# Optimization experiments

Hardware: AMD Instinct MI355X
Metric: run time of the kernel (lower is better)

Reference implementation:

```python
import jax, jax.numpy as jnp
import numpy as np

NUM_GROUPS = 32
EPS = 1e-6


def group_norm(x, gamma, beta):
    # x: [B, C, H, W]; GroupNorm over (channels-in-group, H, W)
    B, C, H, W = x.shape
    xg = x.reshape(B, NUM_GROUPS, C // NUM_GROUPS, H, W)
    mean = xg.mean(axis=(2, 3, 4), keepdims=True)
    var = xg.var(axis=(2, 3, 4), keepdims=True)
    xn = ((xg - mean) * jax.lax.rsqrt(var + EPS)).reshape(B, C, H, W)
    return xn * gamma[None, :, None, None] + beta[None, :, None, None]


def conv1x1(x, w, b):
    # 1x1 conv == channel-mixing matmul. w: [C_out, C_in]
    return jnp.einsum('bchw,oc->bohw', x, w) + b[None, :, None, None]


def setup_inputs() -> dict:
    key = jax.random.key(0)
    ks = jax.random.split(key, 6)
    B, C, H, W = 8, 256, 64, 64
    s = 1.0 / np.sqrt(C)  # fan-in scaled weights (like Conv2d default)
    inp = {
        'x': jax.random.normal(ks[0], (B, C, H, W), jnp.float32),
        'gamma': jnp.ones((C,), jnp.float32),
        'beta': jnp.zeros((C,), jnp.float32),
        'wq': jax.random.normal(ks[1], (C, C), jnp.float32) * s,
        'bq': jnp.zeros((C,), jnp.float32),
        'wk': jax.random.normal(ks[2], (C, C), jnp.float32) * s,
        'bk': jnp.zeros((C,), jnp.float32),
        'wv': jax.random.normal(ks[3], (C, C), jnp.float32) * s,
        'bv': jnp.zeros((C,), jnp.float32),
        'wo': jax.random.normal(ks[4], (C, C), jnp.float32) * s,
        'bo': jnp.zeros((C,), jnp.float32),
    }
    return inp


def reference(x, gamma, beta, wq, bq, wk, bk, wv, bv, wo, bo):
    B, C, H, W = x.shape
    h = group_norm(x, gamma, beta)
    q = conv1x1(h, wq, bq)
    k = conv1x1(h, wk, bk)
    v = conv1x1(h, wv, bv)
    # elu + 1 feature map (nonnegative kernel features)
    q = jax.nn.elu(q) + 1.0
    k = jax.nn.elu(k) + 1.0
    N = H * W
    kf = k.reshape(B, C, N)            # [B, C, N]
    vf = v.reshape(B, C, N)            # [B, C, N]
    qf = q.reshape(B, C, N)            # [B, C, N]
    # kv = k @ v^T : [B, C, C]
    kv = jnp.einsum('bcn,bdn->bcd', kf, vf)
    # h_out[b, n, d] = sum_c q[b, c, n] * kv[b, c, d]; stored channel-first
    h_out = jnp.einsum('bcn,bcd->bdn', qf, kv).reshape(B, C, H, W)
    return x + conv1x1(h_out, wo, bo)
```

## Files before the change

### kernel.cpp

```cpp
#include <hip/hip_runtime.h>
#include <math.h>

#define C_DIM 256
#define N_DIM 4096
#define B_DIM 8

typedef __attribute__((ext_vector_type(8))) short bf16x8;
typedef __attribute__((ext_vector_type(4))) float f32x4;
typedef __attribute__((ext_vector_type(8))) unsigned short us8;
typedef __attribute__((ext_vector_type(4))) unsigned short us4;

__device__ inline unsigned short f2bf(float f) {
    unsigned int u = __float_as_uint(f);
    u += 0x7fffu + ((u >> 16) & 1u);
    return (unsigned short)(u >> 16);
}

__device__ inline void gload_lds16(const void* g, void* l) {
    __builtin_amdgcn_global_load_lds(
        (const __attribute__((address_space(1))) unsigned int*)g,
        (__attribute__((address_space(3))) unsigned int*)l, 16, 0, 0);
}

__global__ __launch_bounds__(256) void prep_kernel(
    const float* __restrict__ wq, const float* __restrict__ wk,
    const float* __restrict__ wv, const float* __restrict__ wo,
    const float* __restrict__ bk, const float* __restrict__ bv,
    const float* __restrict__ x,
    unsigned short* __restrict__ wqb, unsigned short* __restrict__ wkvb,
    unsigned short* __restrict__ wob, float* __restrict__ bkv,
    float2* __restrict__ sums)
{
    int z = blockIdx.x;
    int t = threadIdx.x;
    if (z < 256) {
        const float* s; unsigned short* d;
        int which = z >> 6;
        if (which == 0)      { s = wq; d = wqb; }
        else if (which == 1) { s = wk; d = wkvb; }
        else if (which == 2) { s = wv; d = wkvb + 65536; }
        else                 { s = wo; d = wob; }
        int idx = (z & 63) * 1024 + t * 4;
        float4 v = *(const float4*)(s + idx);
        us4 r; r[0] = f2bf(v.x); r[1] = f2bf(v.y); r[2] = f2bf(v.z); r[3] = f2bf(v.w);
        *(us4*)(d + idx) = r;
    } else if (z == 256) {
        bkv[t]       = bk[t];
        bkv[t + 256] = bv[t];
    } else {
        int bc = z - 257;
        const float* xc = x + (size_t)bc * N_DIM;
        float s = 0.f, q = 0.f;
        for (int i = t; i < 1024; i += 256) {
            float4 v = ((const float4*)xc)[i];
            s += v.x + v.y + v.z + v.w;
            q += v.x*v.x + v.y*v.y + v.z*v.z + v.w*v.w;
        }
        #pragma unroll
        for (int off = 32; off > 0; off >>= 1) {
            s += __shfl_down(s, off);
            q += __shfl_down(q, off);
        }
        __shared__ float red[8];
        int w = t >> 6;
        if ((t & 63) == 0) { red[w*2] = s; red[w*2+1] = q; }
        __syncthreads();
        if (t == 0) {
            sums[bc] = make_float2(red[0]+red[2]+red[4]+red[6],
                                   red[1]+red[3]+red[5]+red[7]);
        }
    }
}

__global__ __launch_bounds__(256) void kvred(const float* __restrict__ src, unsigned short* __restrict__ dst) {
    int gi = (blockIdx.x * 256 + threadIdx.x) * 4;
    int b = gi >> 16, idx = gi & 65535;
    float4 a = make_float4(0.f,0.f,0.f,0.f);
    #pragma unroll
    for (int sp = 0; sp < 8; sp++) {
        float4 v = *(const float4*)(src + (((size_t)b*8 + sp) << 16) + idx);
        a.x += v.x; a.y += v.y; a.z += v.z; a.w += v.w;
    }
    us4 r; r[0] = f2bf(a.x); r[1] = f2bf(a.y); r[2] = f2bf(a.z); r[3] = f2bf(a.w);
    *(us4*)(dst + ((size_t)b << 16) + idx) = r;
}


__device__ __forceinline__ void stage_w(const unsigned short* __restrict__ W,
                                        unsigned short* __restrict__ dst, int kt, int t) {
    #pragma unroll
    for (int s = 0; s < 4; s++) {
        int c = t + s*256;
        int row = c >> 2, slot = c & 3;
        int cs = slot ^ ((row >> 1) & 3);
        gload_lds16(W + (size_t)row*256 + kt + cs*8, dst + c*8);
    }
}

__device__ __forceinline__ void phase_kv(
    const unsigned short* __restrict__ W, const unsigned short* __restrict__ hs,
    unsigned short* __restrict__ wst, unsigned short* __restrict__ kvdst,
    const float* __restrict__ biasr, int ccb, int n0, bool elu, int t)
{
    int w = t >> 6, l = t & 63;
    int wm = w >> 1, wn = w & 1;
    int l15 = l & 15, quad = l >> 4;
    int acol = (quad ^ ((l15 >> 1) & 3)) * 8;
    int rsw  = (l15 >> 1) & 3;

    f32x4 acc[8][2];
    #pragma unroll
    for (int i = 0; i < 8; i++)
        #pragma unroll
        for (int j = 0; j < 2; j++)
            #pragma unroll
            for (int r = 0; r < 4; r++) acc[i][j][r] = 0.f;

    stage_w(W, wst, 0, t);
    asm volatile("s_waitcnt vmcnt(0)" ::: "memory");
    __syncthreads();

    int buf = 0;
    for (int kt = 0; kt < 8; ++kt) {
        if (kt + 1 < 8) stage_w(W, wst + (buf^1)*8192, (kt+1)*32, t);
        __builtin_amdgcn_sched_barrier(0);
        bf16x8 af[8], bfr[2];
        #pragma unroll
        for (int i = 0; i < 8; i++)
            af[i] = *(const bf16x8*)(wst + buf*8192 + (wm*128 + i*16 + l15)*32 + acol);
        #pragma unroll
        for (int j = 0; j < 2; j++) {
            int n = wn*32 + j*16 + l15;
            bfr[j] = *(const bf16x8*)(hs + n*256 + (kt*4 + (quad ^ rsw))*8);
        }
        __builtin_amdgcn_s_setprio(1);
        #pragma unroll
        for (int i = 0; i < 8; i++)
            #pragma unroll
            for (int j = 0; j < 2; j++)
                acc[i][j] = __builtin_amdgcn_mfma_f32_16x16x32_bf16(af[i], bfr[j], acc[i][j], 0, 0, 0);
        __builtin_amdgcn_s_setprio(0);
        __builtin_amdgcn_sched_barrier(0);
        asm volatile("s_waitcnt vmcnt(0)" ::: "memory");
        __syncthreads();
        buf ^= 1;
    }

    unsigned short* ep = wst;
    #pragma unroll
    for (int h = 0; h < 2; h++) {
        if (wm == h) {
            #pragma unroll
            for (int i = 0; i < 8; i++) {
                #pragma unroll
                for (int j = 0; j < 2; j++) {
                    int cl = wn*32 + j*16 + l15;
                    #pragma unroll
                    for (int r = 0; r < 4; r++) {
                        int rloc = i*16 + quad*4 + r;
                        float val = acc[i][j][r] + biasr[h*128 + rloc];
                        if (elu) val = val > 0.f ? val + 1.f : __expf(val);
                        ep[rloc*72 + cl] = f2bf(val);
                    }
                }
            }
        }
        __syncthreads();
        #pragma unroll
        for (int it = 0; it < 4; it++) {
            int idx = t + it*256;
            int row = idx >> 3;
            int colc = (idx & 7) * 8;
            us8 vv = *(us8*)(ep + row*72 + colc);
            *(us8*)(kvdst + (size_t)(ccb + h*128 + row)*4096 + n0 + colc) = vv;
        }
        __syncthreads();
    }
}

__device__ __forceinline__ void phase_q(
    const unsigned short* __restrict__ W, const unsigned short* __restrict__ hs,
    unsigned short* __restrict__ wst, unsigned short* __restrict__ qdst,
    const float* __restrict__ bq, int n0, int t)
{
    int w = t >> 6, l = t & 63;
    int wm = w >> 1, wn = w & 1;
    int l15 = l & 15, quad = l >> 4;
    int acol = (quad ^ ((l15 >> 1) & 3)) * 8;
    int rsw  = (l15 >> 1) & 3;

    f32x4 acc[2][8];
    #pragma unroll
    for (int i = 0; i < 2; i++)
        #pragma unroll
        for (int j = 0; j < 8; j++)
            #pragma unroll
            for (int r = 0; r < 4; r++) acc[i][j][r] = 0.f;

    stage_w(W, wst, 0, t);
    asm volatile("s_waitcnt vmcnt(0)" ::: "memory");
    __syncthreads();

    int buf = 0;
    for (int kt = 0; kt < 8; ++kt) {
        if (kt + 1 < 8) stage_w(W, wst + (buf^1)*8192, (kt+1)*32, t);
        __builtin_amdgcn_sched_barrier(0);
        bf16x8 af[2], bfr[8];
        #pragma unroll
        for (int i = 0; i < 2; i++) {
            int n = wm*32 + i*16 + l15;
            af[i] = *(const bf16x8*)(hs + n*256 + (kt*4 + (quad ^ rsw))*8);
        }
        #pragma unroll
        for (int j = 0; j < 8; j++)
            bfr[j] = *(const bf16x8*)(wst + buf*8192 + (wn*128 + j*16 + l15)*32 + acol);
        __builtin_amdgcn_s_setprio(1);
        #pragma unroll
        for (int i = 0; i < 2; i++)
            #pragma unroll
            for (int j = 0; j < 8; j++)
                acc[i][j] = __builtin_amdgcn_mfma_f32_16x16x32_bf16(af[i], bfr[j], acc[i][j], 0, 0, 0);
        __builtin_amdgcn_s_setprio(0);
        __builtin_amdgcn_sched_barrier(0);
        asm volatile("s_waitcnt vmcnt(0)" ::: "memory");
        __syncthreads();
        buf ^= 1;
    }

    unsigned short* ep = wst;
    #pragma unroll
    for (int h = 0; h < 2; h++) {
        if (wm == h) {
            #pragma unroll
            for (int i = 0; i < 2; i++) {
                #pragma unroll
                for (int j = 0; j < 8; j++) {
                    int cl = wn*128 + j*16 + l15;
                    float bi = bq[cl];
                    #pragma unroll
                    for (int r = 0; r < 4; r++) {
                        int rloc = i*16 + quad*4 + r;
                        float val = acc[i][j][r] + bi;
                        val = val > 0.f ? val + 1.f : __expf(val);
                        ep[rloc*264 + cl] = f2bf(val);
                    }
                }
            }
        }
        __syncthreads();
        #pragma unroll
        for (int it = 0; it < 4; it++) {
            int idx = t + it*256;
            int row = idx >> 5;
            int colc = (idx & 31) * 8;
            us8 vv = *(us8*)(ep + row*264 + colc);
            *(us8*)(qdst + (size_t)(n0 + h*32 + row)*256 + colc) = vv;
        }
        __syncthreads();
    }
}

__global__ __launch_bounds__(256, 2) void fused_qkv(
    const float* __restrict__ x, const float2* __restrict__ sums,
    const float* __restrict__ gamma, const float* __restrict__ beta,
    const unsigned short* __restrict__ wqb, const unsigned short* __restrict__ wkvb,
    const float* __restrict__ bq, const float* __restrict__ bkv,
    unsigned short* __restrict__ qT, unsigned short* __restrict__ kvbuf)
{
    __shared__ __align__(16) unsigned short hs[16384];
    __shared__ __align__(16) unsigned short wst[16384];
    __shared__ float scale[256], shift[256];

    int b  = blockIdx.y;
    int n0 = blockIdx.x * 64;
    int t  = threadIdx.x;

    {
        int c = t, gbase = c & ~7;
        float s = 0.f, q = 0.f;
        #pragma unroll
        for (int j = 0; j < 8; j++) { float2 u = sums[b*256 + gbase + j]; s += u.x; q += u.y; }
        float mean = s * (1.f/32768.f);
        float var  = q * (1.f/32768.f) - mean*mean;
        float inv  = rsqrtf(var + 1e-6f);
        float gm = gamma[c] * inv;
        scale[c] = gm; shift[c] = beta[c] - mean*gm;
    }
    __syncthreads();

    #pragma unroll
    for (int it = 0; it < 8; ++it) {
        int c  = it*32 + (t >> 3);
        int nl = (t & 7) * 8;
        const float* xp = x + ((size_t)(b*256 + c))*4096 + n0 + nl;
        float4 v0 = *(const float4*)xp;
        float4 v1 = *(const float4*)(xp + 4);
        float sc = scale[c], sh = shift[c];
        int chunk = c >> 3, pos = c & 7;
        float vv[8] = {v0.x, v0.y, v0.z, v0.w, v1.x, v1.y, v1.z, v1.w};
        #pragma unroll
        for (int r = 0; r < 8; ++r) {
            int n = nl + r;
            int cs = (chunk & ~3) | ((chunk & 3) ^ ((n >> 1) & 3));
            hs[n*256 + cs*8 + pos] = f2bf(vv[r] * sc + sh);
        }
    }
    __syncthreads();

    unsigned short* kvdst = kvbuf + (size_t)b * 2097152;
    phase_kv(wkvb,         hs, wst, kvdst, bkv,       0,   n0, true,  t);
    phase_kv(wkvb + 65536, hs, wst, kvdst, bkv + 256, 256, n0, false, t);
    phase_q (wqb,          hs, wst, qT + (size_t)b*1048576, bq, n0, t);
}

template<int MODE>
__device__ __forceinline__ void gemm_body(
    const unsigned short* __restrict__ Ab, const unsigned short* __restrict__ Bb,
    const float* __restrict__ bias, const float* __restrict__ residb,
    void* __restrict__ Cb,
    int N, int K, int k0, int Ks, int m_blk, int n_blk, char* smem)
{
    unsigned short* lds = (unsigned short*)smem;

    int t = threadIdx.x;
    int w = t >> 6, l = t & 63;
    int wm = w >> 1, wn = w & 1;
    int l15 = l & 15, quad = l >> 4;

    int srow = w * 16 + (l >> 2);
    int skc  = (((l & 3) ^ ((l >> 3) & 3)) * 8);

    f32x4 acc[4][4];
    #pragma unroll
    for (int i = 0; i < 4; i++)
        #pragma unroll
        for (int j = 0; j < 4; j++)
            #pragma unroll
            for (int r = 0; r < 4; r++) acc[i][j][r] = 0.f;

    auto stage = [&](int buf, int kt) {
        unsigned short* Asl = lds + buf*8192 + t*8;
        unsigned short* Bsl = Asl + 4096;
        #pragma unroll
        for (int rep = 0; rep < 2; rep++) {
            gload_lds16(Ab + (size_t)(m_blk + rep*64 + srow) * K + kt + skc, Asl + rep*2048);
            gload_lds16(Bb + (size_t)(n_blk + rep*64 + srow) * K + kt + skc, Bsl + rep*2048);
        }
    };

    const int nt = Ks >> 5;

    stage(0, k0);
    if (nt > 1) stage(1, k0 + 32);

    int acol = (quad ^ ((l15 >> 1) & 3)) * 8;

    int bufc = 0;
    for (int kt = 0; kt < nt; ++kt) {
        if (kt + 1 < nt) asm volatile("s_waitcnt vmcnt(4)" ::: "memory");
        else             asm volatile("s_waitcnt vmcnt(0)" ::: "memory");
        __builtin_amdgcn_s_barrier();
        __builtin_amdgcn_sched_barrier(0);
        if (kt + 2 < nt) {
            int bufn = bufc + 2; if (bufn >= 3) bufn -= 3;
            stage(bufn, k0 + (kt + 2) * 32);
        }
        __builtin_amdgcn_sched_barrier(0);

        const unsigned short* Aw = lds + bufc*8192 + (wm*64 + l15)*32 + acol;
        const unsigned short* Bw = lds + bufc*8192 + 4096 + (wn*64 + l15)*32 + acol;
        bf16x8 af[4], bfr[4];
        #pragma unroll
        for (int i = 0; i < 4; i++) af[i]  = *(const bf16x8*)(Aw + i*512);
        #pragma unroll
        for (int j = 0; j < 4; j++) bfr[j] = *(const bf16x8*)(Bw + j*512);
        __builtin_amdgcn_s_setprio(1);
        #pragma unroll
        for (int i = 0; i < 4; i++)
            #pragma unroll
            for (int j = 0; j < 4; j++)
                acc[i][j] = __builtin_amdgcn_mfma_f32_16x16x32_bf16(af[i], bfr[j], acc[i][j], 0, 0, 0);
        __builtin_amdgcn_s_setprio(0);
        bufc = (bufc == 2) ? 0 : bufc + 1;
    }
    __syncthreads();

    if (MODE == 4) {
        unsigned short* ep = (unsigned short*)smem;
        unsigned short* Cp = (unsigned short*)Cb;
        #pragma unroll
        for (int h = 0; h < 2; h++) {
            if (wm == h) {
                int row0 = quad*4;
                int col0 = wn*64 + l15;
                #pragma unroll
                for (int i = 0; i < 4; i++)
                    #pragma unroll
                    for (int j = 0; j < 4; j++)
                        #pragma unroll
                        for (int r = 0; r < 4; r++)
                            ep[(row0 + i*16 + r)*136 + col0 + j*16] = f2bf(acc[i][j][r]);
            }
            __syncthreads();
            #pragma unroll
            for (int it = 0; it < 4; it++) {
                int row = it*16 + (t >> 4);
                int col = (t & 15) * 8;
                us8 vv = *(us8*)(ep + row*136 + col);
                *(us8*)(Cp + (size_t)(m_blk + h*64 + row) * N + n_blk + col) = vv;
            }
            __syncthreads();
        }
    } else {
        float* ep32 = (float*)smem;
        float* Cp = (float*)Cb;
        #pragma unroll
        for (int h = 0; h < 2; h++) {
            if (wm == h) {
                int row0 = quad*4;
                int col0 = wn*64 + l15;
                #pragma unroll
                for (int i = 0; i < 4; i++)
                    #pragma unroll
                    for (int j = 0; j < 4; j++)
                        #pragma unroll
                        for (int r = 0; r < 4; r++)
                            ep32[(row0 + i*16 + r)*140 + col0 + j*16] = acc[i][j][r];
            }
            __syncthreads();
            #pragma unroll
            for (int it = 0; it < 8; it++) {
                int rl  = it*8 + (t >> 5);
                int row = m_blk + h*64 + rl;
                int col = (t & 31) * 4;
                f32x4 vv = *(f32x4*)(ep32 + rl*140 + col);
                if (MODE == 5) {
                    float bi = bias[row];
                    float4 rv = *(const float4*)(residb + (size_t)row * N + n_blk + col);
                    vv[0] += bi + rv.x; vv[1] += bi + rv.y;
                    vv[2] += bi + rv.z; vv[3] += bi + rv.w;
                }
                *(f32x4*)(Cp + (size_t)row * N + n_blk + col) = vv;
            }
            __syncthreads();
        }
    }
}

template<int MODE>
__global__ __launch_bounds__(256) void gemm_nt(
    const unsigned short* __restrict__ A, const unsigned short* __restrict__ B,
    const float* __restrict__ bias, const float* __restrict__ resid,
    void* __restrict__ Cout,
    int N, int K, int splits,
    size_t sA, size_t sB, size_t sC, size_t sR, int elem4)
{
    __shared__ __align__(16) char smem[49152];
    int b  = blockIdx.z / splits;
    int sp = blockIdx.z % splits;
    int Ks = K / splits;
    size_t cbase = (MODE == 3) ? ((size_t)(b*splits + sp)) * sC : (size_t)b * sC;
    void* Cb = elem4 ? (void*)((float*)Cout + cbase) : (void*)((unsigned short*)Cout + cbase);
    gemm_body<MODE>(A + b*sA, B + b*sB, bias,
                    resid ? resid + b*sR : nullptr, Cb,
                    N, K, sp*Ks, Ks, blockIdx.y*128, blockIdx.x*128, smem);
}

extern "C" void kernel_launch(void* const* d_in, const int* in_sizes, int n_in,
                              void* d_out, int out_size, void* d_ws, size_t ws_size,
                              hipStream_t stream) {
    const float* x     = (const float*)d_in[0];
    const float* gamma = (const float*)d_in[1];
    const float* beta  = (const float*)d_in[2];
    const float* wq    = (const float*)d_in[3];
    const float* bq    = (const float*)d_in[4];
    const float* wk    = (const float*)d_in[5];
    const float* bk    = (const float*)d_in[6];
    const float* wv    = (const float*)d_in[7];
    const float* bv    = (const float*)d_in[8];
    const float* wo    = (const float*)d_in[9];
    const float* bo    = (const float*)d_in[10];
    float* out = (float*)d_out;

    const size_t TEN = (size_t)B_DIM * C_DIM * N_DIM;
    unsigned short* ws16  = (unsigned short*)d_ws;
    unsigned short* hT    = ws16;
    unsigned short* qT    = hT    + TEN;
    unsigned short* kvbuf = qT    + TEN;
    unsigned short* kvb   = kvbuf + 2*TEN;
    unsigned short* M2b   = kvb   + 524288;
    unsigned short* wqb   = M2b   + 524288;
    unsigned short* wkvb  = wqb   + 65536;
    unsigned short* wob   = wkvb  + 131072;
    float*          bkv   = (float*)(wob + 65536);
    float2*         sums  = (float2*)(bkv + 512);
    float*          kvf   = (float*)(sums + 2048);

    prep_kernel<<<dim3(2305), 256, 0, stream>>>(wq, wk, wv, wo, bk, bv, x,
                                                wqb, wkvb, wob, bkv, sums);
    fused_qkv<<<dim3(N_DIM/64, B_DIM), 256, 0, stream>>>(
        x, sums, gamma, beta, wqb, wkvb, bq, bkv, qT, kvbuf);
    gemm_nt<3><<<dim3(2, 2, B_DIM*8), 256, 0, stream>>>(
        kvbuf, kvbuf + 1048576, nullptr, nullptr, kvf,
        256, 4096, 8, 2097152, 2097152, 65536, 0, 1);
    kvred<<<dim3(512), 256, 0, stream>>>(kvf, kvb);
    gemm_nt<4><<<dim3(2, 2, B_DIM), 256, 0, stream>>>(
        wob, kvb, nullptr, nullptr, M2b,
        256, 256, 1, 0, 65536, 65536, 0, 0);
    gemm_nt<5><<<dim3(32, 2, B_DIM), 256, 0, stream>>>(
        M2b, qT, bo, x, out,
        4096, 256, 1, 65536, 1048576, 1048576, 1048576, 1);
}
```

Baseline: 173.9 us.

## Single-buffer weight staging in fused QKV to cut LDS and raise occupancy

Replaces the double-buffered LDS weight staging in the K/V and Q projection phases with one buffer that is loaded synchronously between k-steps, halving the weight LDS footprint. The hidden-state tile swizzle widens from 4-way to 8-way XOR to reduce bank conflicts, and the Q epilogue now reuses the hidden-state buffer. The first weight tile is prefetched before the group-norm prologue, and the launch_bounds minimum-blocks hint is dropped. The aim is to fit more blocks per CU through lower LDS use, at the cost of losing load/compute overlap inside each block and possibly higher register pressure.

Result: no change. 172.7 us (-0.7%).

```diff
diff --git a/kernel.cpp b/kernel.cpp
--- a/kernel.cpp
+++ b/kernel.cpp
@@ -97,7 +97,7 @@
     }
 }
 
-__device__ __forceinline__ void phase_kv(
+__device__ __forceinline__ void phase_kv2(
     const unsigned short* __restrict__ W, const unsigned short* __restrict__ hs,
     unsigned short* __restrict__ wst, unsigned short* __restrict__ kvdst,
     const float* __restrict__ biasr, int ccb, int n0, bool elu, int t)
@@ -105,8 +105,8 @@
     int w = t >> 6, l = t & 63;
     int wm = w >> 1, wn = w & 1;
     int l15 = l & 15, quad = l >> 4;
-    int acol = (quad ^ ((l15 >> 1) & 3)) * 8;
-    int rsw  = (l15 >> 1) & 3;
+    int wcol = (quad ^ ((l15 >> 1) & 3)) * 8;
+    int rsw8 = (l15 >> 1) & 7;
 
     f32x4 acc[8][2];
     #pragma unroll
@@ -116,22 +116,16 @@
             #pragma unroll
             for (int r = 0; r < 4; r++) acc[i][j][r] = 0.f;
 
-    stage_w(W, wst, 0, t);
-    asm volatile("s_waitcnt vmcnt(0)" ::: "memory");
-    __syncthreads();
-
-    int buf = 0;
     for (int kt = 0; kt < 8; ++kt) {
-        if (kt + 1 < 8) stage_w(W, wst + (buf^1)*8192, (kt+1)*32, t);
-        __builtin_amdgcn_sched_barrier(0);
         bf16x8 af[8], bfr[2];
         #pragma unroll
         for (int i = 0; i < 8; i++)
-            af[i] = *(const bf16x8*)(wst + buf*8192 + (wm*128 + i*16 + l15)*32 + acol);
+            af[i] = *(const bf16x8*)(wst + (wm*128 + i*16 + l15)*32 + wcol);
+        int coff = ((kt & ~1)*4 + (((kt & 1)*4 + quad) ^ rsw8)) * 8;
         #pragma unroll
         for (int j = 0; j < 2; j++) {
             int n = wn*32 + j*16 + l15;
-            bfr[j] = *(const bf16x8*)(hs + n*256 + (kt*4 + (quad ^ rsw))*8);
+            bfr[j] = *(const bf16x8*)(hs + n*256 + coff);
         }
         __builtin_amdgcn_s_setprio(1);
         #pragma unroll
@@ -140,25 +134,28 @@
             for (int j = 0; j < 2; j++)
                 acc[i][j] = __builtin_amdgcn_mfma_f32_16x16x32_bf16(af[i], bfr[j], acc[i][j], 0, 0, 0);
         __builtin_amdgcn_s_setprio(0);
-        __builtin_amdgcn_sched_barrier(0);
-        asm volatile("s_waitcnt vmcnt(0)" ::: "memory");
-        __syncthreads();
-        buf ^= 1;
+        __syncthreads();
+        if (kt < 7) {
+            stage_w(W, wst, (kt+1)*32, t);
+            __syncthreads();
+        }
     }
 
     unsigned short* ep = wst;
     #pragma unroll
-    for (int h = 0; h < 2; h++) {
-        if (wm == h) {
-            #pragma unroll
-            for (int i = 0; i < 8; i++) {
+    for (int rd = 0; rd < 4; ++rd) {
+        int wmsel = rd >> 1, h2 = rd & 1;
+        if (wm == wmsel) {
+            #pragma unroll
+            for (int i2 = 0; i2 < 4; i2++) {
+                int i = h2*4 + i2;
                 #pragma unroll
                 for (int j = 0; j < 2; j++) {
                     int cl = wn*32 + j*16 + l15;
                     #pragma unroll
                     for (int r = 0; r < 4; r++) {
-                        int rloc = i*16 + quad*4 + r;
-                        float val = acc[i][j][r] + biasr[h*128 + rloc];
+                        int rloc = i2*16 + quad*4 + r;
+                        float val = acc[i][j][r] + biasr[wmsel*128 + h2*64 + rloc];
                         if (elu) val = val > 0.f ? val + 1.f : __expf(val);
                         ep[rloc*72 + cl] = f2bf(val);
                     }
@@ -167,27 +164,26 @@
         }
         __syncthreads();
         #pragma unroll
-        for (int it = 0; it < 4; it++) {
+        for (int it = 0; it < 2; it++) {
             int idx = t + it*256;
-            int row = idx >> 3;
-            int colc = (idx & 7) * 8;
+            int row = idx >> 3, colc = (idx & 7) * 8;
             us8 vv = *(us8*)(ep + row*72 + colc);
-            *(us8*)(kvdst + (size_t)(ccb + h*128 + row)*4096 + n0 + colc) = vv;
-        }
-        __syncthreads();
-    }
-}
-
-__device__ __forceinline__ void phase_q(
-    const unsigned short* __restrict__ W, const unsigned short* __restrict__ hs,
+            *(us8*)(kvdst + (size_t)(ccb + wmsel*128 + h2*64 + row)*4096 + n0 + colc) = vv;
+        }
+        __syncthreads();
+    }
+}
+
+__device__ __forceinline__ void phase_q2(
+    const unsigned short* __restrict__ W, unsigned short* __restrict__ hs,
     unsigned short* __restrict__ wst, unsigned short* __restrict__ qdst,
     const float* __restrict__ bq, int n0, int t)
 {
     int w = t >> 6, l = t & 63;
     int wm = w >> 1, wn = w & 1;
     int l15 = l & 15, quad = l >> 4;
-    int acol = (quad ^ ((l15 >> 1) & 3)) * 8;
-    int rsw  = (l15 >> 1) & 3;
+    int wcol = (quad ^ ((l15 >> 1) & 3)) * 8;
+    int rsw8 = (l15 >> 1) & 7;
 
     f32x4 acc[2][8];
     #pragma unroll
@@ -197,23 +193,17 @@
             #pragma unroll
             for (int r = 0; r < 4; r++) acc[i][j][r] = 0.f;
 
-    stage_w(W, wst, 0, t);
-    asm volatile("s_waitcnt vmcnt(0)" ::: "memory");
-    __syncthreads();
-
-    int buf = 0;
     for (int kt = 0; kt < 8; ++kt) {
-        if (kt + 1 < 8) stage_w(W, wst + (buf^1)*8192, (kt+1)*32, t);
-        __builtin_amdgcn_sched_barrier(0);
         bf16x8 af[2], bfr[8];
+        int coff = ((kt & ~1)*4 + (((kt & 1)*4 + quad) ^ rsw8)) * 8;
         #pragma unroll
         for (int i = 0; i < 2; i++) {
             int n = wm*32 + i*16 + l15;
-            af[i] = *(const bf16x8*)(hs + n*256 + (kt*4 + (quad ^ rsw))*8);
+            af[i] = *(const bf16x8*)(hs + n*256 + coff);
         }
         #pragma unroll
         for (int j = 0; j < 8; j++)
-            bfr[j] = *(const bf16x8*)(wst + buf*8192 + (wn*128 + j*16 + l15)*32 + acol);
+            bfr[j] = *(const bf16x8*)(wst + (wn*128 + j*16 + l15)*32 + wcol);
         __builtin_amdgcn_s_setprio(1);
         #pragma unroll
         for (int i = 0; i < 2; i++)
@@ -221,13 +211,14 @@
             for (int j = 0; j < 8; j++)
                 acc[i][j] = __builtin_amdgcn_mfma_f32_16x16x32_bf16(af[i], bfr[j], acc[i][j], 0, 0, 0);
         __builtin_amdgcn_s_setprio(0);
-        __builtin_amdgcn_sched_barrier(0);
-        asm volatile("s_waitcnt vmcnt(0)" ::: "memory");
-        __syncthreads();
-        buf ^= 1;
-    }
-
-    unsigned short* ep = wst;
+        __syncthreads();
+        if (kt < 7) {
+            stage_w(W, wst, (kt+1)*32, t);
+            __syncthreads();
+        }
+    }
+
+    unsigned short* ep = hs;
     #pragma unroll
     for (int h = 0; h < 2; h++) {
         if (wm == h) {
@@ -260,7 +251,7 @@
     }
 }
 
-__global__ __launch_bounds__(256, 2) void fused_qkv(
+__global__ __launch_bounds__(256) void fused_qkv(
     const float* __restrict__ x, const float2* __restrict__ sums,
     const float* __restrict__ gamma, const float* __restrict__ beta,
     const unsigned short* __restrict__ wqb, const unsigned short* __restrict__ wkvb,
@@ -268,12 +259,14 @@
     unsigned short* __restrict__ qT, unsigned short* __restrict__ kvbuf)
 {
     __shared__ __align__(16) unsigned short hs[16384];
-    __shared__ __align__(16) unsigned short wst[16384];
+    __shared__ __align__(16) unsigned short wst[8192];
     __shared__ float scale[256], shift[256];
 
     int b  = blockIdx.y;
     int n0 = blockIdx.x * 64;
     int t  = threadIdx.x;
+
+    stage_w(wkvb, wst, 0, t);
 
     {
         int c = t, gbase = c & ~7;
@@ -301,16 +294,20 @@
         #pragma unroll
         for (int r = 0; r < 8; ++r) {
             int n = nl + r;
-            int cs = (chunk & ~3) | ((chunk & 3) ^ ((n >> 1) & 3));
+            int cs = (chunk & ~7) | ((chunk & 7) ^ ((n >> 1) & 7));
             hs[n*256 + cs*8 + pos] = f2bf(vv[r] * sc + sh);
         }
     }
     __syncthreads();
 
     unsigned short* kvdst = kvbuf + (size_t)b * 2097152;
-    phase_kv(wkvb,         hs, wst, kvdst, bkv,       0,   n0, true,  t);
-    phase_kv(wkvb + 65536, hs, wst, kvdst, bkv + 256, 256, n0, false, t);
-    phase_q (wqb,          hs, wst, qT + (size_t)b*1048576, bq, n0, t);
+    phase_kv2(wkvb,         hs, wst, kvdst, bkv,       0,   n0, true,  t);
+    stage_w(wkvb + 65536, wst, 0, t);
+    __syncthreads();
+    phase_kv2(wkvb + 65536, hs, wst, kvdst, bkv + 256, 256, n0, false, t);
+    stage_w(wqb, wst, 0, t);
+    __syncthreads();
+    phase_q2(wqb, hs, wst, qT + (size_t)b*1048576, bq, n0, t);
 }
 
 template<int MODE>
```
